# Kernel tuning notes

Hardware: AMD Instinct MI355X
Metric: run time of the kernel (lower is better)

The kernel has to match this reference:

```python
import jax, jax.numpy as jnp
import numpy as np

EPS = 1e-5
R = 3


def _layernorm(x, gamma, beta):
    mu = jnp.mean(x, axis=-1, keepdims=True)
    var = jnp.mean(jnp.square(x - mu), axis=-1, keepdims=True)
    return (x - mu) * jax.lax.rsqrt(var + EPS) * gamma + beta


def setup_inputs() -> dict:
    key = jax.random.key(0)
    ks = jax.random.split(key, 16)
    N, C, H, W = 32, 256, 32, 32
    ic = C // 2
    L = H * W
    R2 = R * R
    d_attn = R2 * L        # 9216
    d_out = ic * L         # 131072
    return {
        "x": jax.random.normal(ks[0], (N, C, H, W), jnp.float32),
        "wq": jax.random.normal(ks[1], (ic, C), jnp.float32) / np.sqrt(C),
        "wk": jax.random.normal(ks[2], (ic, C), jnp.float32) / np.sqrt(C),
        "gamma1": jnp.ones((d_attn,), jnp.float32),
        "beta1": jnp.zeros((d_attn,), jnp.float32),
        "w1": jax.random.normal(ks[3], (C, d_attn), jnp.float32) / np.sqrt(d_attn),
        "b1": jnp.zeros((C,), jnp.float32),
        "w2": jax.random.normal(ks[4], (d_out, C), jnp.float32) / np.sqrt(C),
        "b2": jnp.zeros((d_out,), jnp.float32),
        "gamma2": jnp.ones((d_out,), jnp.float32),
        "beta2": jnp.zeros((d_out,), jnp.float32),
        "w_out": jax.random.normal(ks[5], (C, ic), jnp.float32) / np.sqrt(ic),
        "bn_gamma": jax.random.normal(ks[6], (C,), jnp.float32),
        "bn_beta": jax.random.normal(ks[7], (C,), jnp.float32),
        "bn_mean": jax.random.normal(ks[8], (C,), jnp.float32),
        "bn_var": jax.random.uniform(ks[9], (C,), jnp.float32, 0.5, 1.5),
    }


def reference(x, wq, wk, gamma1, beta1, w1, b1, w2, b2, gamma2, beta2,
              w_out, bn_gamma, bn_beta, bn_mean, bn_var):
    N, C, H, W = x.shape
    ic = wq.shape[0]
    L = H * W
    R2 = R * R
    pad = (R - 1) // 2

    # 1x1 convs == channel GEMMs
    q = jnp.einsum('nchw,oc->nohw', x, wq).reshape(N, ic, L)       # [N,ic,L]
    k = jnp.einsum('nchw,oc->nohw', x, wk)                          # [N,ic,H,W]

    # unfold: RxR local patches, torch channel-major ordering [ic, R2]
    kp = jnp.pad(k, ((0, 0), (0, 0), (pad, pad), (pad, pad)))
    patches = jnp.stack([kp[:, :, i:i + H, j:j + W]
                         for i in range(R) for j in range(R)], axis=-1)
    patches = patches.reshape(N, ic, L, R2)                         # [N,ic,L,R2]

    # local attention scores: q . k over channels at each spatial loc
    f = jnp.einsum('ncl,nclr->nlr', q, patches)                     # [N,L,R2]
    f = f.transpose(0, 2, 1).reshape(N, R2 * L)                     # [N, R2*L]

    # f = f + dropout(f) -> identity at inference => 2f
    f = f + f
    f = _layernorm(f, gamma1, beta1)

    # FFN
    h = jax.nn.relu(f @ w1.T + b1)                                  # [N,C]
    h = h @ w2.T + b2                                               # [N, ic*L]
    h = _layernorm(h, gamma2, beta2)
    y = h.reshape(N, ic, H, W)

    # output 1x1 conv + BatchNorm2d (inference mode)
    wy = jnp.einsum('nchw,oc->nohw', y, w_out)                      # [N,C,H,W]
    scale = (bn_gamma * jax.lax.rsqrt(bn_var + EPS))[None, :, None, None]
    wy = (wy - bn_mean[None, :, None, None]) * scale + bn_beta[None, :, None, None]
    return wy + x
```

## Files before the change

kernel.cpp:

```cpp
#include <hip/hip_runtime.h>

#define NN 32
#define CC 256
#define LL 1024
#define IC 128
#define DA 9216
#define DOUT 131072
#define EPSF 1e-5f

typedef __attribute__((ext_vector_type(8))) short short8;
typedef __attribute__((ext_vector_type(4))) float f32x4;

__device__ __forceinline__ ushort bf_rne(float f) {
  union { float f; unsigned u; } v;
  v.f = f;
  unsigned u = v.u;
  u += 0x7FFF + ((u >> 16) & 1);
  return (ushort)(u >> 16);
}

__global__ __launch_bounds__(256) void k_wcvt(const float* __restrict__ wq,
                                              const float* __restrict__ wk,
                                              const float* __restrict__ wo,
                                              ushort* __restrict__ wqkbf,
                                              ushort* __restrict__ wobf) {
  int idx = (blockIdx.x * 256 + threadIdx.x) * 4;
  float4 v;
  if (idx < 32768) v = *(const float4*)(wq + idx);
  else if (idx < 65536) v = *(const float4*)(wk + idx - 32768);
  else v = *(const float4*)(wo + idx - 65536);
  ushort4 o;
  o.x = bf_rne(v.x); o.y = bf_rne(v.y); o.z = bf_rne(v.z); o.w = bf_rne(v.w);
  if (idx < 65536) *(ushort4*)(wqkbf + idx) = o;
  else *(ushort4*)(wobf + idx - 65536) = o;
}

__global__ __launch_bounds__(256, 4) void k_qkx(const float* __restrict__ x,
                                                const ushort* __restrict__ wqkbf,
                                                float* __restrict__ q,
                                                float* __restrict__ k) {
  __shared__ ushort xl[64 * 264];
  int t = threadIdx.x;
  int n = blockIdx.y;
  int l0 = blockIdx.x * 64;
  int lane = t & 63, wv = t >> 6;
  int m16 = lane & 15, kg = lane >> 4;

  {
    int l = t & 63, g = t >> 6;
    const float* xn = x + ((size_t)n * CC) * LL + l0 + l;
#pragma unroll
    for (int i = 0; i < 8; i++) {
      int c8 = (i * 4 + g) * 8;
      union { short8 s; ushort u[8]; } p;
#pragma unroll
      for (int j = 0; j < 8; j++) p.u[j] = bf_rne(xn[(size_t)(c8 + j) * LL]);
      *(short8*)&xl[l * 264 + c8] = p.s;
    }
  }
  __syncthreads();

  f32x4 acc[2][2][4];
#pragma unroll
  for (int mt = 0; mt < 2; mt++)
#pragma unroll
    for (int ms = 0; ms < 2; ms++)
#pragma unroll
      for (int ls = 0; ls < 4; ls++) acc[mt][ms][ls] = (f32x4){0.f, 0.f, 0.f, 0.f};

#pragma unroll
  for (int kc = 0; kc < 8; kc++) {
    short8 a[2][2];
#pragma unroll
    for (int mt = 0; mt < 2; mt++)
#pragma unroll
      for (int ms = 0; ms < 2; ms++)
        a[mt][ms] = *(const short8*)(wqkbf +
            (((mt * 128 + wv * 32 + ms * 16 + m16) << 8) + kc * 32 + kg * 8));
#pragma unroll
    for (int ls = 0; ls < 4; ls++) {
      short8 b = *(const short8*)&xl[(ls * 16 + m16) * 264 + kc * 32 + kg * 8];
      acc[0][0][ls] =
          __builtin_amdgcn_mfma_f32_16x16x32_bf16(a[0][0], b, acc[0][0][ls], 0, 0, 0);
      acc[0][1][ls] =
          __builtin_amdgcn_mfma_f32_16x16x32_bf16(a[0][1], b, acc[0][1][ls], 0, 0, 0);
      acc[1][0][ls] =
          __builtin_amdgcn_mfma_f32_16x16x32_bf16(a[1][0], b, acc[1][0][ls], 0, 0, 0);
      acc[1][1][ls] =
          __builtin_amdgcn_mfma_f32_16x16x32_bf16(a[1][1], b, acc[1][1][ls], 0, 0, 0);
    }
  }

#pragma unroll
  for (int mt = 0; mt < 2; mt++) {
    float* outp = (mt ? k : q) + (size_t)n * IC * LL;
#pragma unroll
    for (int ms = 0; ms < 2; ms++)
#pragma unroll
      for (int ls = 0; ls < 4; ls++) {
        int col = l0 + ls * 16 + m16;
#pragma unroll
        for (int r = 0; r < 4; r++)
          outp[(size_t)(wv * 32 + ms * 16 + kg * 4 + r) * LL + col] =
              acc[mt][ms][ls][r];
      }
  }
}

__global__ __launch_bounds__(256) void k_attn(const float* __restrict__ q,
                                              const float* __restrict__ k,
                                              float* __restrict__ f2) {
  int n = blockIdx.x;
  int c0 = blockIdx.y * 32;
  int l = blockIdx.z * 256 + threadIdx.x;
  int h = l >> 5, w = l & 31;
  const float* qn = q + (size_t)n * IC * LL;
  const float* kn = k + (size_t)n * IC * LL;
  bool val[9];
  int off[9];
#pragma unroll
  for (int i = 0; i < 3; i++)
#pragma unroll
    for (int j = 0; j < 3; j++) {
      int r = i * 3 + j;
      int hh = h + i - 1, ww = w + j - 1;
      val[r] = (hh >= 0 && hh < 32 && ww >= 0 && ww < 32);
      off[r] = hh * 32 + ww;
    }
  float acc[9];
#pragma unroll
  for (int r = 0; r < 9; r++) acc[r] = 0.f;
#pragma unroll 4
  for (int cc = 0; cc < 32; cc++) {
    int c = c0 + cc;
    float qv = qn[c * LL + l];
    const float* kc = kn + c * LL;
#pragma unroll
    for (int r = 0; r < 9; r++) {
      float kv = val[r] ? kc[off[r]] : 0.f;
      acc[r] += qv * kv;
    }
  }
#pragma unroll
  for (int r = 0; r < 9; r++)
    atomicAdd(&f2[(size_t)n * DA + r * LL + l], 2.f * acc[r]);
}

__global__ __launch_bounds__(256) void k_ln1(float* __restrict__ f2,
                                             const float* __restrict__ g1,
                                             const float* __restrict__ b1) {
  int n = blockIdx.x, t = threadIdx.x;
  float* row = f2 + (size_t)n * DA;
  float4 v[9];
  float s = 0.f, ss = 0.f;
#pragma unroll
  for (int kk = 0; kk < 9; kk++) {
    v[kk] = ((const float4*)row)[t + kk * 256];
    s += v[kk].x + v[kk].y + v[kk].z + v[kk].w;
    ss += v[kk].x * v[kk].x + v[kk].y * v[kk].y + v[kk].z * v[kk].z +
          v[kk].w * v[kk].w;
  }
#pragma unroll
  for (int o = 32; o; o >>= 1) {
    s += __shfl_down(s, o);
    ss += __shfl_down(ss, o);
  }
  __shared__ float ps[4], pss[4], stats[2];
  int wid = t >> 6, lid = t & 63;
  if (lid == 0) { ps[wid] = s; pss[wid] = ss; }
  __syncthreads();
  if (t == 0) {
    float S = ps[0] + ps[1] + ps[2] + ps[3];
    float SS = pss[0] + pss[1] + pss[2] + pss[3];
    float mu = S / DA;
    float var = SS / DA - mu * mu;
    stats[0] = mu;
    stats[1] = rsqrtf(var + EPSF);
  }
  __syncthreads();
  float mu = stats[0], rs = stats[1];
#pragma unroll
  for (int kk = 0; kk < 9; kk++) {
    float4 g = ((const float4*)g1)[t + kk * 256];
    float4 b = ((const float4*)b1)[t + kk * 256];
    float4 o;
    o.x = (v[kk].x - mu) * rs * g.x + b.x;
    o.y = (v[kk].y - mu) * rs * g.y + b.y;
    o.z = (v[kk].z - mu) * rs * g.z + b.z;
    o.w = (v[kk].w - mu) * rs * g.w + b.w;
    ((float4*)row)[t + kk * 256] = o;
  }
}

__global__ __launch_bounds__(256) void k_ffn1(const float* __restrict__ fln,
                                              const float* __restrict__ w1,
                                              const float* __restrict__ b1,
                                              ushort* __restrict__ h1bf) {
  int o = blockIdx.x, nsb = blockIdx.y * 8, t = threadIdx.x;
  float acc[8];
#pragma unroll
  for (int i = 0; i < 8; i++) acc[i] = 0.f;
  const float4* w1r = (const float4*)(w1 + (size_t)o * DA);
  for (int kk = 0; kk < 9; kk++) {
    float4 wv = w1r[t + kk * 256];
#pragma unroll
    for (int i = 0; i < 8; i++) {
      float4 fv = ((const float4*)(fln + (size_t)(nsb + i) * DA))[t + kk * 256];
      acc[i] += wv.x * fv.x + wv.y * fv.y + wv.z * fv.z + wv.w * fv.w;
    }
  }
#pragma unroll
  for (int i = 0; i < 8; i++)
#pragma unroll
    for (int s = 32; s; s >>= 1) acc[i] += __shfl_down(acc[i], s);
  __shared__ float part[4][8];
  int wid = t >> 6, lid = t & 63;
  if (lid == 0) {
#pragma unroll
    for (int i = 0; i < 8; i++) part[wid][i] = acc[i];
  }
  __syncthreads();
  if (t < 8) {
    float sum = part[0][t] + part[1][t] + part[2][t] + part[3][t] + b1[o];
    h1bf[(size_t)(nsb + t) * CC + o] = bf_rne(fmaxf(sum, 0.f));
  }
}

__global__ __launch_bounds__(256, 3) void k_ffn2(
    const ushort* __restrict__ h1bf, const float* __restrict__ w2,
    const float* __restrict__ b2, float* __restrict__ h2,
    float* __restrict__ st) {
  __shared__ float bs[64];
  int t = threadIdx.x;
  int lane = t & 63, wv = t >> 6;
  int m16 = lane & 15, kg = lane >> 4;
  int j0 = blockIdx.x * 256 + wv * 64;
  if (t < 64) bs[t] = 0.f;

  int j[4];
#pragma unroll
  for (int nn = 0; nn < 4; nn++) j[nn] = j0 + nn * 16 + m16;

  f32x4 acc[2][4];
#pragma unroll
  for (int m = 0; m < 2; m++)
#pragma unroll
    for (int nn = 0; nn < 4; nn++) acc[m][nn] = (f32x4){0.f, 0.f, 0.f, 0.f};

  float4 lo[4], hi[4];
#pragma unroll
  for (int nn = 0; nn < 4; nn++) {
    const float* src = w2 + (size_t)j[nn] * CC + kg * 8;
    lo[nn] = *(const float4*)src;
    hi[nn] = *(const float4*)(src + 4);
  }

#pragma unroll
  for (int kc = 0; kc < 8; kc++) {
    short8 a0 = *(const short8*)(h1bf + m16 * CC + kc * 32 + kg * 8);
    short8 a1 = *(const short8*)(h1bf + (16 + m16) * CC + kc * 32 + kg * 8);
    short8 bf[4];
#pragma unroll
    for (int nn = 0; nn < 4; nn++) {
      union { short8 s; ushort u[8]; } cv;
      cv.u[0] = bf_rne(lo[nn].x); cv.u[1] = bf_rne(lo[nn].y);
      cv.u[2] = bf_rne(lo[nn].z); cv.u[3] = bf_rne(lo[nn].w);
      cv.u[4] = bf_rne(hi[nn].x); cv.u[5] = bf_rne(hi[nn].y);
      cv.u[6] = bf_rne(hi[nn].z); cv.u[7] = bf_rne(hi[nn].w);
      bf[nn] = cv.s;
    }
    if (kc < 7) {
#pragma unroll
      for (int nn = 0; nn < 4; nn++) {
        const float* src = w2 + (size_t)j[nn] * CC + (kc + 1) * 32 + kg * 8;
        lo[nn] = *(const float4*)src;
        hi[nn] = *(const float4*)(src + 4);
      }
    }
#pragma unroll
    for (int nn = 0; nn < 4; nn++) {
      acc[0][nn] =
          __builtin_amdgcn_mfma_f32_16x16x32_bf16(a0, bf[nn], acc[0][nn], 0, 0, 0);
      acc[1][nn] =
          __builtin_amdgcn_mfma_f32_16x16x32_bf16(a1, bf[nn], acc[1][nn], 0, 0, 0);
    }
  }
  __syncthreads();

  float b2v[4];
#pragma unroll
  for (int nn = 0; nn < 4; nn++) b2v[nn] = b2[j[nn]];

  float s8[2][4], q8[2][4];
#pragma unroll
  for (int m = 0; m < 2; m++)
#pragma unroll
    for (int r = 0; r < 4; r++) { s8[m][r] = 0.f; q8[m][r] = 0.f; }
#pragma unroll
  for (int m = 0; m < 2; m++)
#pragma unroll
    for (int nn = 0; nn < 4; nn++) {
#pragma unroll
      for (int r = 0; r < 4; r++) {
        float v = acc[m][nn][r] + b2v[nn];
        int row = m * 16 + kg * 4 + r;
        h2[(size_t)row * DOUT + j[nn]] = v;
        s8[m][r] += v;
        q8[m][r] += v * v;
      }
    }
#pragma unroll
  for (int off = 8; off; off >>= 1)
#pragma unroll
    for (int m = 0; m < 2; m++)
#pragma unroll
      for (int r = 0; r < 4; r++) {
        s8[m][r] += __shfl_down(s8[m][r], off, 16);
        q8[m][r] += __shfl_down(q8[m][r], off, 16);
      }
  if (m16 == 0) {
#pragma unroll
    for (int m = 0; m < 2; m++)
#pragma unroll
      for (int r = 0; r < 4; r++) {
        int row = m * 16 + kg * 4 + r;
        atomicAdd(&bs[row], s8[m][r]);
        atomicAdd(&bs[32 + row], q8[m][r]);
      }
  }
  __syncthreads();
  if (t < 64) atomicAdd(&st[t], bs[t]);
}

__global__ __launch_bounds__(256, 2) void k_out(
    const float* __restrict__ h2, const float* __restrict__ st,
    const float* __restrict__ g2, const float* __restrict__ b2,
    const ushort* __restrict__ wobf, const float* __restrict__ bn_g,
    const float* __restrict__ bn_b, const float* __restrict__ bn_m,
    const float* __restrict__ bn_v, const float* __restrict__ x,
    float* __restrict__ out) {
  __shared__ ushort yl[64 * 136];
  int t = threadIdx.x;
  int n = blockIdx.y;
  int l0 = blockIdx.x * 64;
  float mu = st[n] * (1.f / DOUT);
  float rs = rsqrtf(st[32 + n] * (1.f / DOUT) - mu * mu + EPSF);

  {
    int l = t & 63, og = t >> 6;
    const float* h2n = h2 + (size_t)n * DOUT;
#pragma unroll
    for (int i = 0; i < 4; i++) {
      int o8 = (i * 4 + og) * 8;
      union { short8 s; ushort u[8]; } p;
#pragma unroll
      for (int jj = 0; jj < 8; jj++) {
        int d = (o8 + jj) * LL + l0 + l;
        float yv = (h2n[d] - mu) * rs * g2[d] + b2[d];
        p.u[jj] = bf_rne(yv);
      }
      *(short8*)&yl[l * 136 + o8] = p.s;
    }
  }
  __syncthreads();

  int lane = t & 63, wv = t >> 6;
  int m16 = lane & 15, kg = lane >> 4;
  f32x4 acc[4][4];
#pragma unroll
  for (int ms = 0; ms < 4; ms++)
#pragma unroll
    for (int ls = 0; ls < 4; ls++) acc[ms][ls] = (f32x4){0.f, 0.f, 0.f, 0.f};

#pragma unroll
  for (int kc = 0; kc < 4; kc++) {
    short8 a[4];
#pragma unroll
    for (int ms = 0; ms < 4; ms++)
      a[ms] = *(const short8*)(wobf +
          (((wv * 64 + ms * 16 + m16) << 7) + kc * 32 + kg * 8));
#pragma unroll
    for (int ls = 0; ls < 4; ls++) {
      short8 b = *(const short8*)&yl[(ls * 16 + m16) * 136 + kc * 32 + kg * 8];
#pragma unroll
      for (int ms = 0; ms < 4; ms++)
        acc[ms][ls] =
            __builtin_amdgcn_mfma_f32_16x16x32_bf16(a[ms], b, acc[ms][ls], 0, 0, 0);
    }
  }

#pragma unroll
  for (int ms = 0; ms < 4; ms++)
#pragma unroll
    for (int r = 0; r < 4; r++) {
      int O = wv * 64 + ms * 16 + kg * 4 + r;
      float sc = bn_g[O] * rsqrtf(bn_v[O] + EPSF);
      float sh = bn_b[O] - bn_m[O] * sc;
#pragma unroll
      for (int ls = 0; ls < 4; ls++) {
        int col = l0 + ls * 16 + m16;
        size_t base = ((size_t)(n * CC + O)) * LL + col;
        out[base] = acc[ms][ls][r] * sc + sh + x[base];
      }
    }
}

extern "C" void kernel_launch(void* const* d_in, const int* in_sizes, int n_in,
                              void* d_out, int out_size, void* d_ws,
                              size_t ws_size, hipStream_t stream) {
  const float* x = (const float*)d_in[0];
  const float* wq = (const float*)d_in[1];
  const float* wk = (const float*)d_in[2];
  const float* gamma1 = (const float*)d_in[3];
  const float* beta1 = (const float*)d_in[4];
  const float* w1 = (const float*)d_in[5];
  const float* b1 = (const float*)d_in[6];
  const float* w2 = (const float*)d_in[7];
  const float* b2 = (const float*)d_in[8];
  const float* gamma2 = (const float*)d_in[9];
  const float* beta2 = (const float*)d_in[10];
  const float* w_out = (const float*)d_in[11];
  const float* bn_g = (const float*)d_in[12];
  const float* bn_b = (const float*)d_in[13];
  const float* bn_m = (const float*)d_in[14];
  const float* bn_v = (const float*)d_in[15];
  float* outp = (float*)d_out;
  float* ws = (float*)d_ws;

  float* qb = ws;
  float* kb = ws + 4194304;
  float* fb = ws + 8388608;
  float* stb = ws + 8683520;
  ushort* h1bfb = (ushort*)(ws + 8683584);
  ushort* wqkbfb = (ushort*)(ws + 8687680);
  ushort* wobfb = (ushort*)(ws + 8720448);
  float* h2b = qb;

  if (ws_size < 8736832ull * sizeof(float)) return;

  hipMemsetAsync(fb, 0, (294912 + 64) * sizeof(float), stream);
  k_wcvt<<<dim3(96), 256, 0, stream>>>(wq, wk, w_out, wqkbfb, wobfb);
  k_qkx<<<dim3(16, 32), 256, 0, stream>>>(x, wqkbfb, qb, kb);
  k_attn<<<dim3(32, 4, 4), 256, 0, stream>>>(qb, kb, fb);
  k_ln1<<<dim3(32), 256, 0, stream>>>(fb, gamma1, beta1);
  k_ffn1<<<dim3(256, 4), 256, 0, stream>>>(fb, w1, b1, h1bfb);
  k_ffn2<<<dim3(512), 256, 0, stream>>>(h1bfb, w2, b2, h2b, stb);
  k_out<<<dim3(16, 32), 256, 0, stream>>>(h2b, stb, gamma2, beta2, wobfb,
                                          bn_g, bn_b, bn_m, bn_v, x, outp);
}
```

Baseline: 333.5 us.

## Fuse memset into weight cast, packed bf16 conversion, retile FFN and output kernels

Replaces the separate hipMemsetAsync with extra blocks in the weight-conversion kernel that zero the attention/stat buffers. Switches float-to-bf16 conversion to a packed perm-based helper (round-half-up instead of round-to-nearest-even). Doubles the batch rows per ffn1 block to halve w1 re-reads, and halves the per-block tile of ffn2 and the output kernel, doubling their grids and raising occupancy bounds. The rounding change alters numerics slightly, and the smaller tiles reduce per-block reuse.

```diff
diff --git a/kernel.cpp b/kernel.cpp
--- a/kernel.cpp
+++ b/kernel.cpp
@@ -19,20 +19,35 @@
   return (ushort)(u >> 16);
 }
 
+__device__ __forceinline__ unsigned bfp2(float lo, float hi) {
+  union { float f; unsigned u; } a, b;
+  a.f = lo; b.f = hi;
+  return __builtin_amdgcn_perm(b.u + 0x8000u, a.u + 0x8000u, 0x07060302u);
+}
+
 __global__ __launch_bounds__(256) void k_wcvt(const float* __restrict__ wq,
                                               const float* __restrict__ wk,
                                               const float* __restrict__ wo,
                                               ushort* __restrict__ wqkbf,
-                                              ushort* __restrict__ wobf) {
-  int idx = (blockIdx.x * 256 + threadIdx.x) * 4;
-  float4 v;
-  if (idx < 32768) v = *(const float4*)(wq + idx);
-  else if (idx < 65536) v = *(const float4*)(wk + idx - 32768);
-  else v = *(const float4*)(wo + idx - 65536);
-  ushort4 o;
-  o.x = bf_rne(v.x); o.y = bf_rne(v.y); o.z = bf_rne(v.z); o.w = bf_rne(v.w);
-  if (idx < 65536) *(ushort4*)(wqkbf + idx) = o;
-  else *(ushort4*)(wobf + idx - 65536) = o;
+                                              ushort* __restrict__ wobf,
+                                              float* __restrict__ fz) {
+  int b = blockIdx.x;
+  if (b < 96) {
+    int idx = (b * 256 + threadIdx.x) * 4;
+    float4 v;
+    if (idx < 32768) v = *(const float4*)(wq + idx);
+    else if (idx < 65536) v = *(const float4*)(wk + idx - 32768);
+    else v = *(const float4*)(wo + idx - 65536);
+    uint2 o;
+    o.x = bfp2(v.x, v.y);
+    o.y = bfp2(v.z, v.w);
+    if (idx < 65536) *(uint2*)(wqkbf + idx) = o;
+    else *(uint2*)(wobf + idx - 65536) = o;
+  } else {
+    int idx = ((b - 96) * 256 + threadIdx.x) * 4;
+    if (idx < 294976)
+      *(float4*)(fz + idx) = make_float4(0.f, 0.f, 0.f, 0.f);
+  }
 }
 
 __global__ __launch_bounds__(256, 4) void k_qkx(const float* __restrict__ x,
@@ -52,9 +67,14 @@
 #pragma unroll
     for (int i = 0; i < 8; i++) {
       int c8 = (i * 4 + g) * 8;
-      union { short8 s; ushort u[8]; } p;
-#pragma unroll
-      for (int j = 0; j < 8; j++) p.u[j] = bf_rne(xn[(size_t)(c8 + j) * LL]);
+      float v[8];
+#pragma unroll
+      for (int j = 0; j < 8; j++) v[j] = xn[(size_t)(c8 + j) * LL];
+      union { short8 s; unsigned u[4]; } p;
+      p.u[0] = bfp2(v[0], v[1]);
+      p.u[1] = bfp2(v[2], v[3]);
+      p.u[2] = bfp2(v[4], v[5]);
+      p.u[3] = bfp2(v[6], v[7]);
       *(short8*)&xl[l * 264 + c8] = p.s;
     }
   }
@@ -196,37 +216,37 @@
                                               const float* __restrict__ w1,
                                               const float* __restrict__ b1,
                                               ushort* __restrict__ h1bf) {
-  int o = blockIdx.x, nsb = blockIdx.y * 8, t = threadIdx.x;
-  float acc[8];
-#pragma unroll
-  for (int i = 0; i < 8; i++) acc[i] = 0.f;
+  int o = blockIdx.x, nsb = blockIdx.y * 16, t = threadIdx.x;
+  float acc[16];
+#pragma unroll
+  for (int i = 0; i < 16; i++) acc[i] = 0.f;
   const float4* w1r = (const float4*)(w1 + (size_t)o * DA);
   for (int kk = 0; kk < 9; kk++) {
     float4 wv = w1r[t + kk * 256];
 #pragma unroll
-    for (int i = 0; i < 8; i++) {
+    for (int i = 0; i < 16; i++) {
       float4 fv = ((const float4*)(fln + (size_t)(nsb + i) * DA))[t + kk * 256];
       acc[i] += wv.x * fv.x + wv.y * fv.y + wv.z * fv.z + wv.w * fv.w;
     }
   }
 #pragma unroll
-  for (int i = 0; i < 8; i++)
+  for (int i = 0; i < 16; i++)
 #pragma unroll
     for (int s = 32; s; s >>= 1) acc[i] += __shfl_down(acc[i], s);
-  __shared__ float part[4][8];
+  __shared__ float part[4][16];
   int wid = t >> 6, lid = t & 63;
   if (lid == 0) {
 #pragma unroll
-    for (int i = 0; i < 8; i++) part[wid][i] = acc[i];
-  }
-  __syncthreads();
-  if (t < 8) {
+    for (int i = 0; i < 16; i++) part[wid][i] = acc[i];
+  }
+  __syncthreads();
+  if (t < 16) {
     float sum = part[0][t] + part[1][t] + part[2][t] + part[3][t] + b1[o];
     h1bf[(size_t)(nsb + t) * CC + o] = bf_rne(fmaxf(sum, 0.f));
   }
 }
 
-__global__ __launch_bounds__(256, 3) void k_ffn2(
+__global__ __launch_bounds__(256, 4) void k_ffn2(
     const ushort* __restrict__ h1bf, const float* __restrict__ w2,
     const float* __restrict__ b2, float* __restrict__ h2,
     float* __restrict__ st) {
@@ -234,22 +254,20 @@
   int t = threadIdx.x;
   int lane = t & 63, wv = t >> 6;
   int m16 = lane & 15, kg = lane >> 4;
-  int j0 = blockIdx.x * 256 + wv * 64;
+  int j0 = blockIdx.x * 128 + wv * 32;
   if (t < 64) bs[t] = 0.f;
 
-  int j[4];
-#pragma unroll
-  for (int nn = 0; nn < 4; nn++) j[nn] = j0 + nn * 16 + m16;
-
-  f32x4 acc[2][4];
+  int j[2] = {j0 + m16, j0 + 16 + m16};
+
+  f32x4 acc[2][2];
 #pragma unroll
   for (int m = 0; m < 2; m++)
 #pragma unroll
-    for (int nn = 0; nn < 4; nn++) acc[m][nn] = (f32x4){0.f, 0.f, 0.f, 0.f};
-
-  float4 lo[4], hi[4];
-#pragma unroll
-  for (int nn = 0; nn < 4; nn++) {
+    for (int nn = 0; nn < 2; nn++) acc[m][nn] = (f32x4){0.f, 0.f, 0.f, 0.f};
+
+  float4 lo[2], hi[2];
+#pragma unroll
+  for (int nn = 0; nn < 2; nn++) {
     const float* src = w2 + (size_t)j[nn] * CC + kg * 8;
     lo[nn] = *(const float4*)src;
     hi[nn] = *(const float4*)(src + 4);
@@ -259,26 +277,26 @@
   for (int kc = 0; kc < 8; kc++) {
     short8 a0 = *(const short8*)(h1bf + m16 * CC + kc * 32 + kg * 8);
     short8 a1 = *(const short8*)(h1bf + (16 + m16) * CC + kc * 32 + kg * 8);
-    short8 bf[4];
-#pragma unroll
-    for (int nn = 0; nn < 4; nn++) {
-      union { short8 s; ushort u[8]; } cv;
-      cv.u[0] = bf_rne(lo[nn].x); cv.u[1] = bf_rne(lo[nn].y);
-      cv.u[2] = bf_rne(lo[nn].z); cv.u[3] = bf_rne(lo[nn].w);
-      cv.u[4] = bf_rne(hi[nn].x); cv.u[5] = bf_rne(hi[nn].y);
-      cv.u[6] = bf_rne(hi[nn].z); cv.u[7] = bf_rne(hi[nn].w);
+    short8 bf[2];
+#pragma unroll
+    for (int nn = 0; nn < 2; nn++) {
+      union { short8 s; unsigned u[4]; } cv;
+      cv.u[0] = bfp2(lo[nn].x, lo[nn].y);
+      cv.u[1] = bfp2(lo[nn].z, lo[nn].w);
+      cv.u[2] = bfp2(hi[nn].x, hi[nn].y);
+      cv.u[3] = bfp2(hi[nn].z, hi[nn].w);
       bf[nn] = cv.s;
     }
     if (kc < 7) {
 #pragma unroll
-      for (int nn = 0; nn < 4; nn++) {
+      for (int nn = 0; nn < 2; nn++) {
         const float* src = w2 + (size_t)j[nn] * CC + (kc + 1) * 32 + kg * 8;
         lo[nn] = *(const float4*)src;
         hi[nn] = *(const float4*)(src + 4);
       }
     }
 #pragma unroll
-    for (int nn = 0; nn < 4; nn++) {
+    for (int nn = 0; nn < 2; nn++) {
       acc[0][nn] =
           __builtin_amdgcn_mfma_f32_16x16x32_bf16(a0, bf[nn], acc[0][nn], 0, 0, 0);
       acc[1][nn] =
@@ -287,9 +305,7 @@
   }
   __syncthreads();
 
-  float b2v[4];
-#pragma unroll
-  for (int nn = 0; nn < 4; nn++) b2v[nn] = b2[j[nn]];
+  float b2v[2] = {b2[j[0]], b2[j[1]]};
 
   float s8[2][4], q8[2][4];
 #pragma unroll
@@ -299,7 +315,7 @@
 #pragma unroll
   for (int m = 0; m < 2; m++)
 #pragma unroll
-    for (int nn = 0; nn < 4; nn++) {
+    for (int nn = 0; nn < 2; nn++) {
 #pragma unroll
       for (int r = 0; r < 4; r++) {
         float v = acc[m][nn][r] + b2v[nn];
@@ -332,60 +348,64 @@
   if (t < 64) atomicAdd(&st[t], bs[t]);
 }
 
-__global__ __launch_bounds__(256, 2) void k_out(
+__global__ __launch_bounds__(256, 4) void k_out(
     const float* __restrict__ h2, const float* __restrict__ st,
     const float* __restrict__ g2, const float* __restrict__ b2,
     const ushort* __restrict__ wobf, const float* __restrict__ bn_g,
     const float* __restrict__ bn_b, const float* __restrict__ bn_m,
     const float* __restrict__ bn_v, const float* __restrict__ x,
     float* __restrict__ out) {
-  __shared__ ushort yl[64 * 136];
+  __shared__ ushort yl[32 * 136];
   int t = threadIdx.x;
   int n = blockIdx.y;
-  int l0 = blockIdx.x * 64;
+  int l0 = blockIdx.x * 32;
   float mu = st[n] * (1.f / DOUT);
   float rs = rsqrtf(st[32 + n] * (1.f / DOUT) - mu * mu + EPSF);
 
   {
-    int l = t & 63, og = t >> 6;
+    int l = t & 31, og = t >> 5;
     const float* h2n = h2 + (size_t)n * DOUT;
 #pragma unroll
-    for (int i = 0; i < 4; i++) {
-      int o8 = (i * 4 + og) * 8;
-      union { short8 s; ushort u[8]; } p;
+    for (int half = 0; half < 2; half++) {
+      float y[8];
 #pragma unroll
       for (int jj = 0; jj < 8; jj++) {
-        int d = (o8 + jj) * LL + l0 + l;
-        float yv = (h2n[d] - mu) * rs * g2[d] + b2[d];
-        p.u[jj] = bf_rne(yv);
-      }
-      *(short8*)&yl[l * 136 + o8] = p.s;
+        int o = og * 16 + half * 8 + jj;
+        int d = o * LL + l0 + l;
+        y[jj] = (h2n[d] - mu) * rs * g2[d] + b2[d];
+      }
+      union { short8 s; unsigned u[4]; } p;
+      p.u[0] = bfp2(y[0], y[1]);
+      p.u[1] = bfp2(y[2], y[3]);
+      p.u[2] = bfp2(y[4], y[5]);
+      p.u[3] = bfp2(y[6], y[7]);
+      *(short8*)&yl[l * 136 + og * 16 + half * 8] = p.s;
     }
   }
   __syncthreads();
 
   int lane = t & 63, wv = t >> 6;
   int m16 = lane & 15, kg = lane >> 4;
-  f32x4 acc[4][4];
+  f32x4 acc[4][2];
 #pragma unroll
   for (int ms = 0; ms < 4; ms++)
 #pragma unroll
-    for (int ls = 0; ls < 4; ls++) acc[ms][ls] = (f32x4){0.f, 0.f, 0.f, 0.f};
+    for (int ls = 0; ls < 2; ls++) acc[ms][ls] = (f32x4){0.f, 0.f, 0.f, 0.f};
 
 #pragma unroll
   for (int kc = 0; kc < 4; kc++) {
-    short8 a[4];
-#pragma unroll
-    for (int ms = 0; ms < 4; ms++)
-      a[ms] = *(const short8*)(wobf +
+    short8 b[2];
+#pragma unroll
+    for (int ls = 0; ls < 2; ls++)
+      b[ls] = *(const short8*)&yl[(ls * 16 + m16) * 136 + kc * 32 + kg * 8];
+#pragma unroll
+    for (int ms = 0; ms < 4; ms++) {
+      short8 a = *(const short8*)(wobf +
           (((wv * 64 + ms * 16 + m16) << 7) + kc * 32 + kg * 8));
 #pragma unroll
-    for (int ls = 0; ls < 4; ls++) {
-      short8 b = *(const short8*)&yl[(ls * 16 + m16) * 136 + kc * 32 + kg * 8];
-#pragma unroll
-      for (int ms = 0; ms < 4; ms++)
+      for (int ls = 0; ls < 2; ls++)
         acc[ms][ls] =
-            __builtin_amdgcn_mfma_f32_16x16x32_bf16(a[ms], b, acc[ms][ls], 0, 0, 0);
+            __builtin_amdgcn_mfma_f32_16x16x32_bf16(a, b[ls], acc[ms][ls], 0, 0, 0);
     }
   }
 
@@ -397,7 +417,7 @@
       float sc = bn_g[O] * rsqrtf(bn_v[O] + EPSF);
       float sh = bn_b[O] - bn_m[O] * sc;
 #pragma unroll
-      for (int ls = 0; ls < 4; ls++) {
+      for (int ls = 0; ls < 2; ls++) {
         int col = l0 + ls * 16 + m16;
         size_t base = ((size_t)(n * CC + O)) * LL + col;
         out[base] = acc[ms][ls][r] * sc + sh + x[base];
@@ -438,13 +458,12 @@
 
   if (ws_size < 8736832ull * sizeof(float)) return;
 
-  hipMemsetAsync(fb, 0, (294912 + 64) * sizeof(float), stream);
-  k_wcvt<<<dim3(96), 256, 0, stream>>>(wq, wk, w_out, wqkbfb, wobfb);
+  k_wcvt<<<dim3(385), 256, 0, stream>>>(wq, wk, w_out, wqkbfb, wobfb, fb);
   k_qkx<<<dim3(16, 32), 256, 0, stream>>>(x, wqkbfb, qb, kb);
   k_attn<<<dim3(32, 4, 4), 256, 0, stream>>>(qb, kb, fb);
   k_ln1<<<dim3(32), 256, 0, stream>>>(fb, gamma1, beta1);
-  k_ffn1<<<dim3(256, 4), 256, 0, stream>>>(fb, w1, b1, h1bfb);
-  k_ffn2<<<dim3(512), 256, 0, stream>>>(h1bfb, w2, b2, h2b, stb);
-  k_out<<<dim3(16, 32), 256, 0, stream>>>(h2b, stb, gamma2, beta2, wobfb,
+  k_ffn1<<<dim3(256, 2), 256, 0, stream>>>(fb, w1, b1, h1bfb);
+  k_ffn2<<<dim3(1024), 256, 0, stream>>>(h1bfb, w2, b2, h2b, stb);
+  k_out<<<dim3(32, 32), 256, 0, stream>>>(h2b, stb, gamma2, beta2, wobfb,
                                           bn_g, bn_b, bn_m, bn_v, x, outp);
 }
```

Result: slower. 345.1 us (+3.5%).
